# Performance work log

Hardware: AMD Instinct MI355X
Metric: run time of the kernel (lower is better)

The kernel has to match this reference:

```python
import jax, jax.numpy as jnp
import numpy as np

TAU = 0.95
COEF = 0.5
LOG_CLAMP = -100.0  # torch BCELoss clamps log terms at -100


def setup_inputs() -> dict:
    key = jax.random.key(0)
    k1, k2, k3, k4, k5 = jax.random.split(key, 5)
    B, L = 4096, 2048
    eps = 1e-4
    # probabilities in (eps, 1-eps) so log / log1p are finite
    def prob(k, shape):
        return jax.random.uniform(k, shape, dtype=jnp.float32, minval=eps, maxval=1.0 - eps)
    truncation_output = prob(k1, (B, L, 1))
    view_1_output = prob(k2, (B, L, 1))
    view_2_output = prob(k3, (B, L, 1))
    view_3_output = prob(k4, (B, L, 1))
    labels = (jax.random.uniform(k5, (B, L)) < 0.1).astype(jnp.float32)
    return {
        "truncation_output": truncation_output,
        "view_1_output": view_1_output,
        "view_2_output": view_2_output,
        "view_3_output": view_3_output,
        "labels": labels,
    }


def _bce_div_batch(p, y):
    # nn.BCELoss() (mean reduction) then .div(batch_size)
    logp = jnp.maximum(jnp.log(p), LOG_CLAMP)
    log1mp = jnp.maximum(jnp.log1p(-p), LOG_CLAMP)
    bce = -jnp.mean(y * logp + (1.0 - y) * log1mp)
    return bce / p.shape[0]


def _f1_matrix(labels):
    # r[i, j] = F1(labels[i], cutoff=j+1), vectorized via cumsum
    B, L = labels.shape
    cum = jnp.cumsum(labels, axis=1)                       # rel@(j+1)
    k = jnp.arange(1, L + 1, dtype=labels.dtype)           # cutoff
    total = cum[:, -1:]                                    # total relevant per row
    # P = cum/k, R = cum/total -> F1 = 2*cum/(k+total); 0 when no hits
    return jnp.where(cum > 0, 2.0 * cum / (k + total), 0.0)


def reference(truncation_output, view_1_output, view_2_output, view_3_output, labels):
    B = truncation_output.shape[0]
    v1 = _bce_div_batch(view_1_output[..., 0], labels)
    v2 = _bce_div_batch(view_2_output[..., 0], labels)
    v3 = _bce_div_batch(view_3_output[..., 0], labels)

    r = _f1_matrix(labels)                                 # [B, L]
    q = jax.nn.softmax(r / TAU, axis=-1)                   # softmax over list dim
    log_out = jnp.log(truncation_output[..., 0] / TAU)
    trunc_loss = -jnp.sum(log_out * q) / B

    return COEF * trunc_loss + (1.0 - COEF) * (v1 + v2 + v3)
```

## Files before the change

kernel.cpp:

```cpp
#include <hip/hip_runtime.h>

#define B_DIM 4096
#define L_DIM 2048
#define TPB   256
#define RPB   4
#define NW    4
#define NBLK  (B_DIM / RPB)
#define TAU_INV 1.0526315789473684f
#define LOG_TAU_INV 0.05129329438755058f

typedef float v4f __attribute__((ext_vector_type(4)));

__device__ __forceinline__ v4f ntload(const float* p) {
    return __builtin_nontemporal_load((const v4f*)p);
}

__global__ __launch_bounds__(TPB) void milecut_row_kernel(
    const float* __restrict__ trunc,
    const float* __restrict__ view1,
    const float* __restrict__ view2,
    const float* __restrict__ view3,
    const float* __restrict__ labels,
    float* __restrict__ partials)
{
    const int t    = threadIdx.x;
    const int lane = t & 63;
    const int wv   = t >> 6;
    const int row0 = blockIdx.x * RPB;

    __shared__ unsigned swtot[NW];
    __shared__ float    srow[RPB][NW][2];
    __shared__ float    sbce[NW];

    size_t off = (size_t)row0 * L_DIM;
    v4f nya = ntload(labels + off + 4 * t);
    v4f nyb = ntload(labels + off + 4 * (t + 256));
    v4f nta = ntload(trunc  + off + 4 * t);
    v4f ntb = ntload(trunc  + off + 4 * (t + 256));
    v4f n1a = ntload(view1  + off + 4 * t);
    v4f n1b = ntload(view1  + off + 4 * (t + 256));
    v4f n2a = ntload(view2  + off + 4 * t);
    v4f n2b = ntload(view2  + off + 4 * (t + 256));
    v4f n3a = ntload(view3  + off + 4 * t);
    v4f n3b = ntload(view3  + off + 4 * (t + 256));

    float bce = 0.f;

    #pragma unroll
    for (int rr = 0; rr < RPB; ++rr) {
        v4f ya = nya, yb = nyb, ta = nta, tb = ntb;
        v4f u1a = n1a, u1b = n1b, u2a = n2a, u2b = n2b, u3a = n3a, u3b = n3b;
        if (rr + 1 < RPB) {
            size_t o2 = (size_t)(row0 + rr + 1) * L_DIM;
            nya = ntload(labels + o2 + 4 * t);
            nyb = ntload(labels + o2 + 4 * (t + 256));
            nta = ntload(trunc  + o2 + 4 * t);
            ntb = ntload(trunc  + o2 + 4 * (t + 256));
            n1a = ntload(view1  + o2 + 4 * t);
            n1b = ntload(view1  + o2 + 4 * (t + 256));
            n2a = ntload(view2  + o2 + 4 * t);
            n2b = ntload(view2  + o2 + 4 * (t + 256));
            n3a = ntload(view3  + o2 + 4 * t);
            n3b = ntload(view3  + o2 + 4 * (t + 256));
        }

        unsigned m1 = (ya.x > 0.5f ? 1u : 0u) | (ya.y > 0.5f ? 2u : 0u)
                    | (ya.z > 0.5f ? 4u : 0u) | (ya.w > 0.5f ? 8u : 0u);
        unsigned m2 = (yb.x > 0.5f ? 1u : 0u) | (yb.y > 0.5f ? 2u : 0u)
                    | (yb.z > 0.5f ? 4u : 0u) | (yb.w > 0.5f ? 8u : 0u);
        unsigned pv = (unsigned)__popc(m1) | ((unsigned)__popc(m2) << 16);

        unsigned incl = pv;
        #pragma unroll
        for (int o = 1; o < 64; o <<= 1) {
            unsigned n = (unsigned)__shfl_up((int)incl, o, 64);
            if (lane >= o) incl += n;
        }
        if (lane == 63) swtot[wv] = incl;
        __syncthreads();
        unsigned pref = 0, tot = 0;
        #pragma unroll
        for (int w = 0; w < NW; ++w) {
            unsigned x = swtot[w];
            if (w < wv) pref += x;
            tot += x;
        }
        __syncthreads();

        unsigned eo    = incl - pv;
        unsigned excl1 = (pref & 0xffffu) + (eo & 0xffffu);
        unsigned tot1  = tot & 0xffffu;
        unsigned excl2 = tot1 + (pref >> 16) + (eo >> 16);
        float ftotal   = (float)(tot1 + (tot >> 16));

        float esum = 0.f, wtr = 0.f;
        float tva[4] = {ta.x, ta.y, ta.z, ta.w};
        float tvb[4] = {tb.x, tb.y, tb.z, tb.w};
        float w1a[4] = {u1a.x, u1a.y, u1a.z, u1a.w};
        float w1b[4] = {u1b.x, u1b.y, u1b.z, u1b.w};
        float w2a[4] = {u2a.x, u2a.y, u2a.z, u2a.w};
        float w2b[4] = {u2b.x, u2b.y, u2b.z, u2b.w};
        float w3a[4] = {u3a.x, u3a.y, u3a.z, u3a.w};
        float w3b[4] = {u3b.x, u3b.y, u3b.z, u3b.w};
        const float two_tauinv = 2.0f * TAU_INV;
        #pragma unroll
        for (int j = 0; j < 4; ++j) {
            unsigned c1 = excl1 + (unsigned)__popc(m1 & ((2u << j) - 1u));
            unsigned c2 = excl2 + (unsigned)__popc(m2 & ((2u << j) - 1u));
            float d1 = (float)(4 * t + j + 1) + ftotal;
            float d2 = (float)(1024 + 4 * t + j + 1) + ftotal;
            float e1 = __expf(two_tauinv * (float)c1 * __builtin_amdgcn_rcpf(d1));
            float e2 = __expf(two_tauinv * (float)c2 * __builtin_amdgcn_rcpf(d2));
            esum += e1 + e2;
            wtr  += __logf(tva[j]) * e1 + __logf(tvb[j]) * e2;
            bool p1 = (m1 >> j) & 1u;
            bool p2 = (m2 >> j) & 1u;
            float q1 = p1 ? w1a[j] : 1.f - w1a[j];
            float q2 = p1 ? w2a[j] : 1.f - w2a[j];
            float q3 = p1 ? w3a[j] : 1.f - w3a[j];
            float q4 = p2 ? w1b[j] : 1.f - w1b[j];
            float q5 = p2 ? w2b[j] : 1.f - w2b[j];
            float q6 = p2 ? w3b[j] : 1.f - w3b[j];
            bce += __logf(((q1 * q2) * (q3 * q4)) * (q5 * q6));
        }
        wtr += LOG_TAU_INV * esum;

        #pragma unroll
        for (int o = 32; o > 0; o >>= 1) {
            esum += __shfl_down(esum, o, 64);
            wtr  += __shfl_down(wtr,  o, 64);
        }
        if (lane == 0) { srow[rr][wv][0] = esum; srow[rr][wv][1] = wtr; }
    }

    #pragma unroll
    for (int o = 32; o > 0; o >>= 1) bce += __shfl_down(bce, o, 64);
    if (lane == 0) sbce[wv] = bce;
    __syncthreads();
    if (t == 0) {
        float btot = sbce[0] + sbce[1] + sbce[2] + sbce[3];
        float atr = 0.f;
        #pragma unroll
        for (int rr = 0; rr < RPB; ++rr) {
            float es = srow[rr][0][0] + srow[rr][1][0] + srow[rr][2][0] + srow[rr][3][0];
            float wt = srow[rr][0][1] + srow[rr][1][1] + srow[rr][2][1] + srow[rr][3][1];
            atr += wt / es;
        }
        partials[blockIdx.x]        = atr;
        partials[NBLK + blockIdx.x] = btot;
    }
}

__global__ __launch_bounds__(TPB) void milecut_final_kernel(
    const float* __restrict__ partials, float* __restrict__ out)
{
    const int t = threadIdx.x;
    const float4* p4 = (const float4*)partials;
    float4 a = p4[t];
    float4 b = p4[256 + t];
    float st = (a.x + a.y) + (a.z + a.w);
    float sb = (b.x + b.y) + (b.z + b.w);
    #pragma unroll
    for (int o = 32; o > 0; o >>= 1) {
        st += __shfl_down(st, o, 64);
        sb += __shfl_down(sb, o, 64);
    }
    __shared__ float s1[NW], s2[NW];
    const int lane = t & 63, wv = t >> 6;
    if (lane == 0) { s1[wv] = st; s2[wv] = sb; }
    __syncthreads();
    if (t == 0) {
        double St = 0.0, Sb = 0.0;
        #pragma unroll
        for (int w = 0; w < NW; ++w) { St += (double)s1[w]; Sb += (double)s2[w]; }
        double trunc_loss = -St / (double)B_DIM;
        double vsum = -Sb / ((double)B_DIM * (double)L_DIM * (double)B_DIM);
        out[0] = (float)(0.5 * trunc_loss + 0.5 * vsum);
    }
}

extern "C" void kernel_launch(void* const* d_in, const int* in_sizes, int n_in,
                              void* d_out, int out_size, void* d_ws, size_t ws_size,
                              hipStream_t stream) {
    const float* trunc  = (const float*)d_in[0];
    const float* v1     = (const float*)d_in[1];
    const float* v2     = (const float*)d_in[2];
    const float* v3     = (const float*)d_in[3];
    const float* labels = (const float*)d_in[4];

    float* partials = (float*)d_ws;

    milecut_row_kernel<<<NBLK, TPB, 0, stream>>>(trunc, v1, v2, v3, labels, partials);
    milecut_final_kernel<<<1, TPB, 0, stream>>>(partials, (float*)d_out);
}
```

Baseline: 163.0 us.

## Assign one row per wavefront to remove block-level scan barriers

Each wavefront now handles a whole row instead of the block splitting each row across four waves. The prefix scan of label counts runs four interleaved wave-level scans combined with shuffles, which removes the per-row __syncthreads and shared-memory exchange. Loads are software-pipelined across four column chunks within the row. This raises register pressure per thread and holds more loads in flight per wave, which may reduce occupancy.

Result: no change. 164.1 us (+0.7%).

```diff
diff --git a/kernel.cpp b/kernel.cpp
--- a/kernel.cpp
+++ b/kernel.cpp
@@ -3,9 +3,8 @@
 #define B_DIM 4096
 #define L_DIM 2048
 #define TPB   256
-#define RPB   4
 #define NW    4
-#define NBLK  (B_DIM / RPB)
+#define NBLK  1024
 #define TAU_INV 1.0526315789473684f
 #define LOG_TAU_INV 0.05129329438755058f
 
@@ -13,6 +12,11 @@
 
 __device__ __forceinline__ v4f ntload(const float* p) {
     return __builtin_nontemporal_load((const v4f*)p);
+}
+
+__device__ __forceinline__ unsigned nib(v4f y) {
+    return (y.x > 0.5f ? 1u : 0u) | (y.y > 0.5f ? 2u : 0u)
+         | (y.z > 0.5f ? 4u : 0u) | (y.w > 0.5f ? 8u : 0u);
 }
 
 __global__ __launch_bounds__(TPB) void milecut_row_kernel(
@@ -26,128 +30,134 @@
     const int t    = threadIdx.x;
     const int lane = t & 63;
     const int wv   = t >> 6;
-    const int row0 = blockIdx.x * RPB;
-
-    __shared__ unsigned swtot[NW];
-    __shared__ float    srow[RPB][NW][2];
-    __shared__ float    sbce[NW];
-
-    size_t off = (size_t)row0 * L_DIM;
-    v4f nya = ntload(labels + off + 4 * t);
-    v4f nyb = ntload(labels + off + 4 * (t + 256));
-    v4f nta = ntload(trunc  + off + 4 * t);
-    v4f ntb = ntload(trunc  + off + 4 * (t + 256));
-    v4f n1a = ntload(view1  + off + 4 * t);
-    v4f n1b = ntload(view1  + off + 4 * (t + 256));
-    v4f n2a = ntload(view2  + off + 4 * t);
-    v4f n2b = ntload(view2  + off + 4 * (t + 256));
-    v4f n3a = ntload(view3  + off + 4 * t);
-    v4f n3b = ntload(view3  + off + 4 * (t + 256));
-
-    float bce = 0.f;
-
+    const int row  = blockIdx.x * NW + wv;
+
+    __shared__ float srow[NW];
+    __shared__ float sbce[NW];
+
+    const size_t base = (size_t)row * L_DIM + 4 * lane;
+    const float* Lp = labels + base;
+    const float* Tp = trunc  + base;
+    const float* P1 = view1  + base;
+    const float* P2 = view2  + base;
+    const float* P3 = view3  + base;
+
+    v4f yA0 = ntload(Lp);        v4f yA1 = ntload(Lp + 256);
+    v4f yA2 = ntload(Lp + 512);  v4f yA3 = ntload(Lp + 768);
+    v4f yB0 = ntload(Lp + 1024); v4f yB1 = ntload(Lp + 1280);
+    v4f yB2 = ntload(Lp + 1536); v4f yB3 = ntload(Lp + 1792);
+
+    v4f tA  = ntload(Tp);        v4f tB  = ntload(Tp + 1024);
+    v4f a1  = ntload(P1);        v4f b1  = ntload(P1 + 1024);
+    v4f a2  = ntload(P2);        v4f b2  = ntload(P2 + 1024);
+    v4f a3  = ntload(P3);        v4f b3  = ntload(P3 + 1024);
+
+    unsigned mA0 = nib(yA0), mA1 = nib(yA1), mA2 = nib(yA2), mA3 = nib(yA3);
+    unsigned mB0 = nib(yB0), mB1 = nib(yB1), mB2 = nib(yB2), mB3 = nib(yB3);
+
+    unsigned pv0 = (unsigned)__popc(mA0) | ((unsigned)__popc(mB0) << 16);
+    unsigned pv1 = (unsigned)__popc(mA1) | ((unsigned)__popc(mB1) << 16);
+    unsigned pv2 = (unsigned)__popc(mA2) | ((unsigned)__popc(mB2) << 16);
+    unsigned pv3 = (unsigned)__popc(mA3) | ((unsigned)__popc(mB3) << 16);
+
+    unsigned i0 = pv0, i1 = pv1, i2 = pv2, i3 = pv3;
     #pragma unroll
-    for (int rr = 0; rr < RPB; ++rr) {
-        v4f ya = nya, yb = nyb, ta = nta, tb = ntb;
-        v4f u1a = n1a, u1b = n1b, u2a = n2a, u2b = n2b, u3a = n3a, u3b = n3b;
-        if (rr + 1 < RPB) {
-            size_t o2 = (size_t)(row0 + rr + 1) * L_DIM;
-            nya = ntload(labels + o2 + 4 * t);
-            nyb = ntload(labels + o2 + 4 * (t + 256));
-            nta = ntload(trunc  + o2 + 4 * t);
-            ntb = ntload(trunc  + o2 + 4 * (t + 256));
-            n1a = ntload(view1  + o2 + 4 * t);
-            n1b = ntload(view1  + o2 + 4 * (t + 256));
-            n2a = ntload(view2  + o2 + 4 * t);
-            n2b = ntload(view2  + o2 + 4 * (t + 256));
-            n3a = ntload(view3  + o2 + 4 * t);
-            n3b = ntload(view3  + o2 + 4 * (t + 256));
-        }
-
-        unsigned m1 = (ya.x > 0.5f ? 1u : 0u) | (ya.y > 0.5f ? 2u : 0u)
-                    | (ya.z > 0.5f ? 4u : 0u) | (ya.w > 0.5f ? 8u : 0u);
-        unsigned m2 = (yb.x > 0.5f ? 1u : 0u) | (yb.y > 0.5f ? 2u : 0u)
-                    | (yb.z > 0.5f ? 4u : 0u) | (yb.w > 0.5f ? 8u : 0u);
-        unsigned pv = (unsigned)__popc(m1) | ((unsigned)__popc(m2) << 16);
-
-        unsigned incl = pv;
-        #pragma unroll
-        for (int o = 1; o < 64; o <<= 1) {
-            unsigned n = (unsigned)__shfl_up((int)incl, o, 64);
-            if (lane >= o) incl += n;
-        }
-        if (lane == 63) swtot[wv] = incl;
-        __syncthreads();
-        unsigned pref = 0, tot = 0;
-        #pragma unroll
-        for (int w = 0; w < NW; ++w) {
-            unsigned x = swtot[w];
-            if (w < wv) pref += x;
-            tot += x;
-        }
-        __syncthreads();
-
-        unsigned eo    = incl - pv;
-        unsigned excl1 = (pref & 0xffffu) + (eo & 0xffffu);
-        unsigned tot1  = tot & 0xffffu;
-        unsigned excl2 = tot1 + (pref >> 16) + (eo >> 16);
-        float ftotal   = (float)(tot1 + (tot >> 16));
-
-        float esum = 0.f, wtr = 0.f;
-        float tva[4] = {ta.x, ta.y, ta.z, ta.w};
-        float tvb[4] = {tb.x, tb.y, tb.z, tb.w};
-        float w1a[4] = {u1a.x, u1a.y, u1a.z, u1a.w};
-        float w1b[4] = {u1b.x, u1b.y, u1b.z, u1b.w};
-        float w2a[4] = {u2a.x, u2a.y, u2a.z, u2a.w};
-        float w2b[4] = {u2b.x, u2b.y, u2b.z, u2b.w};
-        float w3a[4] = {u3a.x, u3a.y, u3a.z, u3a.w};
-        float w3b[4] = {u3b.x, u3b.y, u3b.z, u3b.w};
-        const float two_tauinv = 2.0f * TAU_INV;
-        #pragma unroll
-        for (int j = 0; j < 4; ++j) {
-            unsigned c1 = excl1 + (unsigned)__popc(m1 & ((2u << j) - 1u));
-            unsigned c2 = excl2 + (unsigned)__popc(m2 & ((2u << j) - 1u));
-            float d1 = (float)(4 * t + j + 1) + ftotal;
-            float d2 = (float)(1024 + 4 * t + j + 1) + ftotal;
-            float e1 = __expf(two_tauinv * (float)c1 * __builtin_amdgcn_rcpf(d1));
-            float e2 = __expf(two_tauinv * (float)c2 * __builtin_amdgcn_rcpf(d2));
-            esum += e1 + e2;
-            wtr  += __logf(tva[j]) * e1 + __logf(tvb[j]) * e2;
-            bool p1 = (m1 >> j) & 1u;
-            bool p2 = (m2 >> j) & 1u;
-            float q1 = p1 ? w1a[j] : 1.f - w1a[j];
-            float q2 = p1 ? w2a[j] : 1.f - w2a[j];
-            float q3 = p1 ? w3a[j] : 1.f - w3a[j];
-            float q4 = p2 ? w1b[j] : 1.f - w1b[j];
-            float q5 = p2 ? w2b[j] : 1.f - w2b[j];
-            float q6 = p2 ? w3b[j] : 1.f - w3b[j];
-            bce += __logf(((q1 * q2) * (q3 * q4)) * (q5 * q6));
-        }
-        wtr += LOG_TAU_INV * esum;
-
-        #pragma unroll
-        for (int o = 32; o > 0; o >>= 1) {
-            esum += __shfl_down(esum, o, 64);
-            wtr  += __shfl_down(wtr,  o, 64);
-        }
-        if (lane == 0) { srow[rr][wv][0] = esum; srow[rr][wv][1] = wtr; }
-    }
-
+    for (int o = 1; o < 64; o <<= 1) {
+        unsigned n0 = (unsigned)__shfl_up((int)i0, o, 64);
+        unsigned n1 = (unsigned)__shfl_up((int)i1, o, 64);
+        unsigned n2 = (unsigned)__shfl_up((int)i2, o, 64);
+        unsigned n3 = (unsigned)__shfl_up((int)i3, o, 64);
+        if (lane >= o) { i0 += n0; i1 += n1; i2 += n2; i3 += n3; }
+    }
+    unsigned tp0 = (unsigned)__shfl((int)i0, 63, 64);
+    unsigned tp1 = (unsigned)__shfl((int)i1, 63, 64);
+    unsigned tp2 = (unsigned)__shfl((int)i2, 63, 64);
+    unsigned tp3 = (unsigned)__shfl((int)i3, 63, 64);
+
+    unsigned e0 = i0 - pv0, e1 = i1 - pv1, e2 = i2 - pv2, e3 = i3 - pv3;
+    unsigned gA0 = tp0 & 0xffffu, gA1 = tp1 & 0xffffu, gA2 = tp2 & 0xffffu, gA3 = tp3 & 0xffffu;
+    unsigned gB0 = tp0 >> 16,     gB1 = tp1 >> 16,     gB2 = tp2 >> 16,     gB3 = tp3 >> 16;
+    unsigned hA = gA0 + gA1 + gA2 + gA3;
+    float ftotal = (float)(hA + gB0 + gB1 + gB2 + gB3);
+
+    unsigned cbA0 =                    (e0 & 0xffffu);
+    unsigned cbA1 = gA0 +              (e1 & 0xffffu);
+    unsigned cbA2 = gA0 + gA1 +        (e2 & 0xffffu);
+    unsigned cbA3 = gA0 + gA1 + gA2 +  (e3 & 0xffffu);
+    unsigned cbB0 = hA +                     (e0 >> 16);
+    unsigned cbB1 = hA + gB0 +               (e1 >> 16);
+    unsigned cbB2 = hA + gB0 + gB1 +         (e2 >> 16);
+    unsigned cbB3 = hA + gB0 + gB1 + gB2 +   (e3 >> 16);
+
+    float esum = 0.f, wtr = 0.f, bce = 0.f;
+    const float two_tauinv = 2.0f * TAU_INV;
+
+#define COMPUTE(MAn, MBn, CBA, CBB, IDXBASE, TA, TB, W1A, W1B, W2A, W2B, W3A, W3B) \
+    do {                                                                       \
+        float tva[4] = {(TA).x, (TA).y, (TA).z, (TA).w};                       \
+        float tvb[4] = {(TB).x, (TB).y, (TB).z, (TB).w};                       \
+        float w1a[4] = {(W1A).x, (W1A).y, (W1A).z, (W1A).w};                   \
+        float w1b[4] = {(W1B).x, (W1B).y, (W1B).z, (W1B).w};                   \
+        float w2a[4] = {(W2A).x, (W2A).y, (W2A).z, (W2A).w};                   \
+        float w2b[4] = {(W2B).x, (W2B).y, (W2B).z, (W2B).w};                   \
+        float w3a[4] = {(W3A).x, (W3A).y, (W3A).z, (W3A).w};                   \
+        float w3b[4] = {(W3B).x, (W3B).y, (W3B).z, (W3B).w};                   \
+        _Pragma("unroll")                                                      \
+        for (int j = 0; j < 4; ++j) {                                          \
+            unsigned c1 = (CBA) + (unsigned)__popc((MAn) & ((2u << j) - 1u));  \
+            unsigned c2 = (CBB) + (unsigned)__popc((MBn) & ((2u << j) - 1u));  \
+            float d1 = (float)((IDXBASE) + j + 1) + ftotal;                    \
+            float d2 = d1 + 1024.0f;                                           \
+            float e1f = __expf(two_tauinv * (float)c1 * __builtin_amdgcn_rcpf(d1)); \
+            float e2f = __expf(two_tauinv * (float)c2 * __builtin_amdgcn_rcpf(d2)); \
+            esum += e1f + e2f;                                                 \
+            wtr  += __logf(tva[j]) * e1f + __logf(tvb[j]) * e2f;               \
+            bool p1 = ((MAn) >> j) & 1u;                                       \
+            bool p2 = ((MBn) >> j) & 1u;                                       \
+            float q1 = p1 ? w1a[j] : 1.f - w1a[j];                             \
+            float q2 = p1 ? w2a[j] : 1.f - w2a[j];                             \
+            float q3 = p1 ? w3a[j] : 1.f - w3a[j];                             \
+            float q4 = p2 ? w1b[j] : 1.f - w1b[j];                             \
+            float q5 = p2 ? w2b[j] : 1.f - w2b[j];                             \
+            float q6 = p2 ? w3b[j] : 1.f - w3b[j];                             \
+            bce += __logf(((q1 * q2) * (q3 * q4)) * (q5 * q6));                \
+        }                                                                      \
+    } while (0)
+
+    v4f ntA = ntload(Tp + 256);  v4f ntB = ntload(Tp + 1280);
+    v4f na1 = ntload(P1 + 256);  v4f nb1 = ntload(P1 + 1280);
+    v4f na2 = ntload(P2 + 256);  v4f nb2 = ntload(P2 + 1280);
+    v4f na3 = ntload(P3 + 256);  v4f nb3 = ntload(P3 + 1280);
+    COMPUTE(mA0, mB0, cbA0, cbB0, 4 * lane, tA, tB, a1, b1, a2, b2, a3, b3);
+
+    tA = ntload(Tp + 512);  tB = ntload(Tp + 1536);
+    a1 = ntload(P1 + 512);  b1 = ntload(P1 + 1536);
+    a2 = ntload(P2 + 512);  b2 = ntload(P2 + 1536);
+    a3 = ntload(P3 + 512);  b3 = ntload(P3 + 1536);
+    COMPUTE(mA1, mB1, cbA1, cbB1, 256 + 4 * lane, ntA, ntB, na1, nb1, na2, nb2, na3, nb3);
+
+    ntA = ntload(Tp + 768);  ntB = ntload(Tp + 1792);
+    na1 = ntload(P1 + 768);  nb1 = ntload(P1 + 1792);
+    na2 = ntload(P2 + 768);  nb2 = ntload(P2 + 1792);
+    na3 = ntload(P3 + 768);  nb3 = ntload(P3 + 1792);
+    COMPUTE(mA2, mB2, cbA2, cbB2, 512 + 4 * lane, tA, tB, a1, b1, a2, b2, a3, b3);
+
+    COMPUTE(mA3, mB3, cbA3, cbB3, 768 + 4 * lane, ntA, ntB, na1, nb1, na2, nb2, na3, nb3);
+
+#undef COMPUTE
+
+    wtr += LOG_TAU_INV * esum;
     #pragma unroll
-    for (int o = 32; o > 0; o >>= 1) bce += __shfl_down(bce, o, 64);
-    if (lane == 0) sbce[wv] = bce;
+    for (int o = 32; o > 0; o >>= 1) {
+        esum += __shfl_down(esum, o, 64);
+        wtr  += __shfl_down(wtr,  o, 64);
+        bce  += __shfl_down(bce,  o, 64);
+    }
+    if (lane == 0) { srow[wv] = wtr / esum; sbce[wv] = bce; }
     __syncthreads();
     if (t == 0) {
-        float btot = sbce[0] + sbce[1] + sbce[2] + sbce[3];
-        float atr = 0.f;
-        #pragma unroll
-        for (int rr = 0; rr < RPB; ++rr) {
-            float es = srow[rr][0][0] + srow[rr][1][0] + srow[rr][2][0] + srow[rr][3][0];
-            float wt = srow[rr][0][1] + srow[rr][1][1] + srow[rr][2][1] + srow[rr][3][1];
-            atr += wt / es;
-        }
-        partials[blockIdx.x]        = atr;
-        partials[NBLK + blockIdx.x] = btot;
+        partials[blockIdx.x]        = srow[0] + srow[1] + srow[2] + srow[3];
+        partials[NBLK + blockIdx.x] = sbce[0] + sbce[1] + sbce[2] + sbce[3];
     }
 }
 
```

## Process one row per block with wave-contiguous segments instead of four rows per block

Applied to the files above, without the earlier changes.

Launches one block per row (4096 blocks) instead of four rows per block with software prefetch of the next row. Each wave now owns a contiguous 512-element half-segment so the two 16-bit scan halves are combined per wave. This drops one barrier per row and the loop-carried register prefetch. In exchange it gives up the explicit next-row prefetch overlap and doubles the final kernel's reduction work.

After: 162.1 us. No clear change (-0.6%).

```diff
diff --git a/kernel.cpp b/kernel.cpp
--- a/kernel.cpp
+++ b/kernel.cpp
@@ -3,9 +3,8 @@
 #define B_DIM 4096
 #define L_DIM 2048
 #define TPB   256
-#define RPB   4
 #define NW    4
-#define NBLK  (B_DIM / RPB)
+#define NBLK  B_DIM
 #define TAU_INV 1.0526315789473684f
 #define LOG_TAU_INV 0.05129329438755058f
 
@@ -13,6 +12,11 @@
 
 __device__ __forceinline__ v4f ntload(const float* p) {
     return __builtin_nontemporal_load((const v4f*)p);
+}
+
+__device__ __forceinline__ unsigned nib(v4f y) {
+    return (y.x > 0.5f ? 1u : 0u) | (y.y > 0.5f ? 2u : 0u)
+         | (y.z > 0.5f ? 4u : 0u) | (y.w > 0.5f ? 8u : 0u);
 }
 
 __global__ __launch_bounds__(TPB) void milecut_row_kernel(
@@ -26,128 +30,95 @@
     const int t    = threadIdx.x;
     const int lane = t & 63;
     const int wv   = t >> 6;
-    const int row0 = blockIdx.x * RPB;
+    const int row  = blockIdx.x;
 
     __shared__ unsigned swtot[NW];
-    __shared__ float    srow[RPB][NW][2];
-    __shared__ float    sbce[NW];
+    __shared__ float    sred[NW][3];
 
-    size_t off = (size_t)row0 * L_DIM;
-    v4f nya = ntload(labels + off + 4 * t);
-    v4f nyb = ntload(labels + off + 4 * (t + 256));
-    v4f nta = ntload(trunc  + off + 4 * t);
-    v4f ntb = ntload(trunc  + off + 4 * (t + 256));
-    v4f n1a = ntload(view1  + off + 4 * t);
-    v4f n1b = ntload(view1  + off + 4 * (t + 256));
-    v4f n2a = ntload(view2  + off + 4 * t);
-    v4f n2b = ntload(view2  + off + 4 * (t + 256));
-    v4f n3a = ntload(view3  + off + 4 * t);
-    v4f n3b = ntload(view3  + off + 4 * (t + 256));
+    const size_t base = (size_t)row * L_DIM + (size_t)(wv << 9) + 4 * lane;
+    const float* Lp = labels + base;
+    const float* Tp = trunc  + base;
+    const float* P1 = view1  + base;
+    const float* P2 = view2  + base;
+    const float* P3 = view3  + base;
 
-    float bce = 0.f;
+    v4f y0  = ntload(Lp);        v4f y1  = ntload(Lp + 256);
+    v4f t0  = ntload(Tp);        v4f t1  = ntload(Tp + 256);
+    v4f w10 = ntload(P1);        v4f w11 = ntload(P1 + 256);
+    v4f w20 = ntload(P2);        v4f w21 = ntload(P2 + 256);
+    v4f w30 = ntload(P3);        v4f w31 = ntload(P3 + 256);
+
+    unsigned m0 = nib(y0), m1 = nib(y1);
+    unsigned pv = (unsigned)__popc(m0) | ((unsigned)__popc(m1) << 16);
+    unsigned incl = pv;
+    #pragma unroll
+    for (int o = 1; o < 64; o <<= 1) {
+        unsigned n = (unsigned)__shfl_up((int)incl, o, 64);
+        if (lane >= o) incl += n;
+    }
+    if (lane == 63) swtot[wv] = incl;
+    __syncthreads();
+
+    unsigned prefix = 0, total = 0, ownA = swtot[wv] & 0xffffu;
+    #pragma unroll
+    for (int w = 0; w < NW; ++w) {
+        unsigned x = swtot[w];
+        unsigned s = (x & 0xffffu) + (x >> 16);
+        if (w < wv) prefix += s;
+        total += s;
+    }
+    unsigned eo  = incl - pv;
+    unsigned cb0 = prefix + (eo & 0xffffu);
+    unsigned cb1 = prefix + ownA + (eo >> 16);
+    float ftotal = (float)total;
+
+    float esum = 0.f, wtr = 0.f, bce = 0.f;
+    const float two_tauinv = 2.0f * TAU_INV;
+    float tva[4] = {t0.x,  t0.y,  t0.z,  t0.w};
+    float tvb[4] = {t1.x,  t1.y,  t1.z,  t1.w};
+    float q1a[4] = {w10.x, w10.y, w10.z, w10.w};
+    float q1b[4] = {w11.x, w11.y, w11.z, w11.w};
+    float q2a[4] = {w20.x, w20.y, w20.z, w20.w};
+    float q2b[4] = {w21.x, w21.y, w21.z, w21.w};
+    float q3a[4] = {w30.x, w30.y, w30.z, w30.w};
+    float q3b[4] = {w31.x, w31.y, w31.z, w31.w};
+    const float dbase = (float)((wv << 9) + 4 * lane + 1) + ftotal;
+    #pragma unroll
+    for (int j = 0; j < 4; ++j) {
+        unsigned c1 = cb0 + (unsigned)__popc(m0 & ((2u << j) - 1u));
+        unsigned c2 = cb1 + (unsigned)__popc(m1 & ((2u << j) - 1u));
+        float d1 = dbase + (float)j;
+        float d2 = d1 + 256.0f;
+        float e1 = __expf(two_tauinv * (float)c1 * __builtin_amdgcn_rcpf(d1));
+        float e2 = __expf(two_tauinv * (float)c2 * __builtin_amdgcn_rcpf(d2));
+        esum += e1 + e2;
+        wtr  += __logf(tva[j]) * e1 + __logf(tvb[j]) * e2;
+        bool p1 = (m0 >> j) & 1u;
+        bool p2 = (m1 >> j) & 1u;
+        float f1 = p1 ? q1a[j] : 1.f - q1a[j];
+        float f2 = p1 ? q2a[j] : 1.f - q2a[j];
+        float f3 = p1 ? q3a[j] : 1.f - q3a[j];
+        float f4 = p2 ? q1b[j] : 1.f - q1b[j];
+        float f5 = p2 ? q2b[j] : 1.f - q2b[j];
+        float f6 = p2 ? q3b[j] : 1.f - q3b[j];
+        bce += __logf(((f1 * f2) * (f3 * f4)) * (f5 * f6));
+    }
+    wtr += LOG_TAU_INV * esum;
 
     #pragma unroll
-    for (int rr = 0; rr < RPB; ++rr) {
-        v4f ya = nya, yb = nyb, ta = nta, tb = ntb;
-        v4f u1a = n1a, u1b = n1b, u2a = n2a, u2b = n2b, u3a = n3a, u3b = n3b;
-        if (rr + 1 < RPB) {
-            size_t o2 = (size_t)(row0 + rr + 1) * L_DIM;
-            nya = ntload(labels + o2 + 4 * t);
-            nyb = ntload(labels + o2 + 4 * (t + 256));
-            nta = ntload(trunc  + o2 + 4 * t);
-            ntb = ntload(trunc  + o2 + 4 * (t + 256));
-            n1a = ntload(view1  + o2 + 4 * t);
-            n1b = ntload(view1  + o2 + 4 * (t + 256));
-            n2a = ntload(view2  + o2 + 4 * t);
-            n2b = ntload(view2  + o2 + 4 * (t + 256));
-            n3a = ntload(view3  + o2 + 4 * t);
-            n3b = ntload(view3  + o2 + 4 * (t + 256));
-        }
-
-        unsigned m1 = (ya.x > 0.5f ? 1u : 0u) | (ya.y > 0.5f ? 2u : 0u)
-                    | (ya.z > 0.5f ? 4u : 0u) | (ya.w > 0.5f ? 8u : 0u);
-        unsigned m2 = (yb.x > 0.5f ? 1u : 0u) | (yb.y > 0.5f ? 2u : 0u)
-                    | (yb.z > 0.5f ? 4u : 0u) | (yb.w > 0.5f ? 8u : 0u);
-        unsigned pv = (unsigned)__popc(m1) | ((unsigned)__popc(m2) << 16);
-
-        unsigned incl = pv;
-        #pragma unroll
-        for (int o = 1; o < 64; o <<= 1) {
-            unsigned n = (unsigned)__shfl_up((int)incl, o, 64);
-            if (lane >= o) incl += n;
-        }
-        if (lane == 63) swtot[wv] = incl;
-        __syncthreads();
-        unsigned pref = 0, tot = 0;
-        #pragma unroll
-        for (int w = 0; w < NW; ++w) {
-            unsigned x = swtot[w];
-            if (w < wv) pref += x;
-            tot += x;
-        }
-        __syncthreads();
-
-        unsigned eo    = incl - pv;
-        unsigned excl1 = (pref & 0xffffu) + (eo & 0xffffu);
-        unsigned tot1  = tot & 0xffffu;
-        unsigned excl2 = tot1 + (pref >> 16) + (eo >> 16);
-        float ftotal   = (float)(tot1 + (tot >> 16));
-
-        float esum = 0.f, wtr = 0.f;
-        float tva[4] = {ta.x, ta.y, ta.z, ta.w};
-        float tvb[4] = {tb.x, tb.y, tb.z, tb.w};
-        float w1a[4] = {u1a.x, u1a.y, u1a.z, u1a.w};
-        float w1b[4] = {u1b.x, u1b.y, u1b.z, u1b.w};
-        float w2a[4] = {u2a.x, u2a.y, u2a.z, u2a.w};
-        float w2b[4] = {u2b.x, u2b.y, u2b.z, u2b.w};
-        float w3a[4] = {u3a.x, u3a.y, u3a.z, u3a.w};
-        float w3b[4] = {u3b.x, u3b.y, u3b.z, u3b.w};
-        const float two_tauinv = 2.0f * TAU_INV;
-        #pragma unroll
-        for (int j = 0; j < 4; ++j) {
-            unsigned c1 = excl1 + (unsigned)__popc(m1 & ((2u << j) - 1u));
-            unsigned c2 = excl2 + (unsigned)__popc(m2 & ((2u << j) - 1u));
-            float d1 = (float)(4 * t + j + 1) + ftotal;
-            float d2 = (float)(1024 + 4 * t + j + 1) + ftotal;
-            float e1 = __expf(two_tauinv * (float)c1 * __builtin_amdgcn_rcpf(d1));
-            float e2 = __expf(two_tauinv * (float)c2 * __builtin_amdgcn_rcpf(d2));
-            esum += e1 + e2;
-            wtr  += __logf(tva[j]) * e1 + __logf(tvb[j]) * e2;
-            bool p1 = (m1 >> j) & 1u;
-            bool p2 = (m2 >> j) & 1u;
-            float q1 = p1 ? w1a[j] : 1.f - w1a[j];
-            float q2 = p1 ? w2a[j] : 1.f - w2a[j];
-            float q3 = p1 ? w3a[j] : 1.f - w3a[j];
-            float q4 = p2 ? w1b[j] : 1.f - w1b[j];
-            float q5 = p2 ? w2b[j] : 1.f - w2b[j];
-            float q6 = p2 ? w3b[j] : 1.f - w3b[j];
-            bce += __logf(((q1 * q2) * (q3 * q4)) * (q5 * q6));
-        }
-        wtr += LOG_TAU_INV * esum;
-
-        #pragma unroll
-        for (int o = 32; o > 0; o >>= 1) {
-            esum += __shfl_down(esum, o, 64);
-            wtr  += __shfl_down(wtr,  o, 64);
-        }
-        if (lane == 0) { srow[rr][wv][0] = esum; srow[rr][wv][1] = wtr; }
+    for (int o = 32; o > 0; o >>= 1) {
+        esum += __shfl_down(esum, o, 64);
+        wtr  += __shfl_down(wtr,  o, 64);
+        bce  += __shfl_down(bce,  o, 64);
     }
-
-    #pragma unroll
-    for (int o = 32; o > 0; o >>= 1) bce += __shfl_down(bce, o, 64);
-    if (lane == 0) sbce[wv] = bce;
+    if (lane == 0) { sred[wv][0] = esum; sred[wv][1] = wtr; sred[wv][2] = bce; }
     __syncthreads();
     if (t == 0) {
-        float btot = sbce[0] + sbce[1] + sbce[2] + sbce[3];
-        float atr = 0.f;
-        #pragma unroll
-        for (int rr = 0; rr < RPB; ++rr) {
-            float es = srow[rr][0][0] + srow[rr][1][0] + srow[rr][2][0] + srow[rr][3][0];
-            float wt = srow[rr][0][1] + srow[rr][1][1] + srow[rr][2][1] + srow[rr][3][1];
-            atr += wt / es;
-        }
-        partials[blockIdx.x]        = atr;
-        partials[NBLK + blockIdx.x] = btot;
+        float es = sred[0][0] + sred[1][0] + sred[2][0] + sred[3][0];
+        float wt = sred[0][1] + sred[1][1] + sred[2][1] + sred[3][1];
+        float bc = sred[0][2] + sred[1][2] + sred[2][2] + sred[3][2];
+        partials[row]        = wt / es;
+        partials[NBLK + row] = bc;
     }
 }
 
@@ -156,10 +127,14 @@
 {
     const int t = threadIdx.x;
     const float4* p4 = (const float4*)partials;
-    float4 a = p4[t];
-    float4 b = p4[256 + t];
-    float st = (a.x + a.y) + (a.z + a.w);
-    float sb = (b.x + b.y) + (b.z + b.w);
+    float st = 0.f, sb = 0.f;
+    #pragma unroll
+    for (int i = 0; i < 4; ++i) {
+        float4 a = p4[t + 256 * i];
+        float4 b = p4[1024 + t + 256 * i];
+        st += (a.x + a.y) + (a.z + a.w);
+        sb += (b.x + b.y) + (b.z + b.w);
+    }
     #pragma unroll
     for (int o = 32; o > 0; o >>= 1) {
         st += __shfl_down(st, o, 64);
```
